# Kernel optimization log

Hardware: AMD Instinct MI355X
Metric: run time of the kernel (lower is better)

## Reference

```python
import jax, jax.numpy as jnp
import numpy as np

N = 100000   # nodes
E = 1200000  # directed edges (avg degree 12)
D = 64       # in_feats
C = 40       # n_classes
K = 16       # propagation steps
ALPHA = 0.05


def setup_inputs() -> dict:
    key = jax.random.key(0)
    k1, k2, k3, k4 = jax.random.split(key, 4)
    feat = jax.random.normal(k1, (N, D), jnp.float32)
    # xavier_uniform for fc.weight [C, D]
    limit = np.sqrt(6.0 / (D + C)).astype(np.float32)
    W = jax.random.uniform(k2, (C, D), jnp.float32, -limit, limit)
    b = jnp.zeros((C,), jnp.float32)
    src = jax.random.randint(k3, (E,), 0, N, dtype=jnp.int32)
    dst = jax.random.randint(k4, (E,), 0, N, dtype=jnp.int32)
    return {"feat": feat, "W": W, "b": b, "src": src, "dst": dst}


def reference(feat, W, b, src, dst):
    # --- getNormAugAdj: A_hat = D^{-1/2} (A + I) D^{-1/2} ---
    loops = jnp.arange(N, dtype=src.dtype)
    row = jnp.concatenate([dst, loops])  # output node of each edge
    col = jnp.concatenate([src, loops])  # input  node of each edge
    ones = jnp.ones(row.shape, feat.dtype)
    deg = jax.ops.segment_sum(ones, row, num_segments=N)  # >= 1 (self-loops)
    dinv = jax.lax.rsqrt(deg)
    w = dinv[row] * dinv[col]  # per-edge normalized weight

    def spmm(x):  # x: [N, D] -> A_hat @ x
        return jax.ops.segment_sum(w[:, None] * x[col], row, num_segments=N)

    feat_ori = feat

    # SSGC loop (faithful to the original, including h /= K inside the loop)
    def step(carry, _):
        x, h = carry
        x = spmm(x)
        h = (h + (1.0 - ALPHA) * x + ALPHA * feat_ori) / K
        return (x, h), None

    (_, h), _ = jax.lax.scan(step, (feat, jnp.zeros_like(feat)), None, length=K)

    # fc(h)
    return h @ W.T + b
```

## Files before the change

kernel.cpp:

```cpp
#include <hip/hip_runtime.h>
#include <hip/hip_fp16.h>

#define NN 100000
#define EE 1200000
#define DD 64
#define CC 40
#define KK 16
#define BSZ 196
#define NBK 512
#define TCAP 3072
#define EPB 4096
#define ABLK ((EE + EPB - 1) / EPB)

#define SLT 261
#define SLT4 196
#define GRID8 (8 * SLT)

typedef int v4i __attribute__((ext_vector_type(4)));

__global__ __launch_bounds__(512) void curinit_kernel(int* __restrict__ cursor) {
    int b = threadIdx.x;
    if (b < NBK) cursor[b] = b * TCAP;
}

__global__ __launch_bounds__(256) void sortA_kernel(const int* __restrict__ src,
                                                    const int* __restrict__ dst,
                                                    int* __restrict__ cursor,
                                                    int2* __restrict__ tmp) {
    __shared__ int2 stg[EPB];
    __shared__ int hist[NBK], loff[NBK], lcur[NBK], gbase[NBK];
    int t = threadIdx.x;
    long e0 = (long)blockIdx.x * EPB;
    int n = (int)((EE - e0 < EPB) ? (EE - e0) : EPB);
    for (int j = t; j < NBK; j += 256) hist[j] = 0;
    __syncthreads();
    int d[16], sx[16];
#pragma unroll
    for (int j = 0; j < 16; ++j) {
        int i = t + j * 256;
        if (i < n) {
            d[j] = dst[e0 + i];
            sx[j] = src[e0 + i];
            atomicAdd(&hist[d[j] / BSZ], 1);
        } else d[j] = -1;
    }
    __syncthreads();
    int c0 = hist[2 * t], c1 = hist[2 * t + 1];
    int s2 = c0 + c1;
    __syncthreads();
    loff[t] = s2;
    __syncthreads();
    for (int off = 1; off < 256; off <<= 1) {
        int u = (t >= off) ? loff[t - off] : 0;
        __syncthreads();
        loff[t] += u;
        __syncthreads();
    }
    int excl = loff[t] - s2;
    __syncthreads();
    loff[2 * t] = excl;          loff[2 * t + 1] = excl + c0;
    lcur[2 * t] = excl;          lcur[2 * t + 1] = excl + c0;
    gbase[2 * t]     = atomicAdd(&cursor[2 * t], c0);
    gbase[2 * t + 1] = atomicAdd(&cursor[2 * t + 1], c1);
    __syncthreads();
#pragma unroll
    for (int j = 0; j < 16; ++j) {
        if (d[j] >= 0) {
            int b = d[j] / BSZ;
            int p = atomicAdd(&lcur[b], 1);
            stg[p] = make_int2(d[j], sx[j]);
        }
    }
    __syncthreads();
    for (int i = t; i < n; i += 256) {
        int2 r = stg[i];
        int b = r.x / BSZ;
        int pos = gbase[b] + (i - loff[b]);
        if (pos < (b + 1) * TCAP) tmp[pos] = r;
    }
}

__global__ __launch_bounds__(512) void bscan_kernel(const int* __restrict__ cursor,
                                                    int* __restrict__ bbase,
                                                    int* __restrict__ row_ptr) {
    __shared__ int sm[512];
    int t = threadIdx.x;
    int v = (t < NBK) ? (cursor[t] - t * TCAP) : 0;
    sm[t] = v;
    __syncthreads();
    for (int off = 1; off < 512; off <<= 1) {
        int u = (t >= off) ? sm[t - off] : 0;
        __syncthreads();
        sm[t] += u;
        __syncthreads();
    }
    if (t < NBK) bbase[t] = sm[t] - v;
    if (t == 511) row_ptr[NN] = sm[511];
}

__global__ __launch_bounds__(256) void sortB_kernel(const int2* __restrict__ tmp,
                                                    const int* __restrict__ cursor,
                                                    const int* __restrict__ bbase,
                                                    float* __restrict__ dinv,
                                                    float* __restrict__ sqd,
                                                    int* __restrict__ row_ptr,
                                                    int* __restrict__ er_src) {
    __shared__ int2 se[TCAP];
    __shared__ int so[TCAP];
    __shared__ int hist[256], lcur[256];
    int b = blockIdx.x;
    int n0 = b * BSZ;
    if (n0 >= NN) return;
    int n1 = n0 + BSZ; if (n1 > NN) n1 = NN;
    int nb = n1 - n0;
    int t = threadIdx.x;
    int cnt = cursor[b] - b * TCAP;
    int base = bbase[b];
    hist[t] = 0;
    __syncthreads();
    for (int i = t; i < cnt; i += 256) {
        int2 r = tmp[b * TCAP + i];
        se[i] = r;
        atomicAdd(&hist[r.x - n0], 1);
    }
    __syncthreads();
    if (t < nb) {
        float dg = (float)(hist[t] + 1);
        dinv[n0 + t] = rsqrtf(dg);
        sqd[n0 + t]  = sqrtf(dg);
    }
    int v = hist[t];
    lcur[t] = v;
    __syncthreads();
    for (int off = 1; off < 256; off <<= 1) {
        int u = (t >= off) ? lcur[t - off] : 0;
        __syncthreads();
        lcur[t] += u;
        __syncthreads();
    }
    int excl = lcur[t] - v;
    __syncthreads();
    lcur[t] = excl;
    if (t < nb) row_ptr[n0 + t] = base + excl;
    __syncthreads();
    for (int i = t; i < cnt; i += 256) {
        int2 r = se[i];
        int ln = r.x - n0;
        int pos = atomicAdd(&lcur[ln], 1);
        so[pos] = r.y;
    }
    __syncthreads();
    for (int i = t; i < cnt; i += 256) er_src[base + i] = so[i];
}

__global__ __launch_bounds__(256) void proj_kernel(const float4* __restrict__ feat4,
                                                   const float* __restrict__ W,
                                                   const float* __restrict__ dinv,
                                                   float4* __restrict__ z0) {
    __shared__ float smW[CC * 68];
    __shared__ float smF[64 * 68];
    __shared__ float smO[64 * 42];
    int t = threadIdx.x;
    for (int j = t; j < CC * 16; j += 256) {
        int c = j >> 4, q = j & 15;
        *(float4*)(smW + c * 68 + q * 4) = ((const float4*)W)[j];
    }
    int n0 = blockIdx.x * 64;
    for (int j = t; j < 64 * 16; j += 256) {
        int r = j >> 4, q = j & 15;
        if (n0 + r < NN)
            *(float4*)(smF + r * 68 + q * 4) = feat4[(size_t)(n0 + r) * 16 + q];
    }
    __syncthreads();
    int ln = t >> 2, c0 = (t & 3) * 10;
    int node = n0 + ln;
    float acc[10];
#pragma unroll
    for (int c = 0; c < 10; ++c) acc[c] = 0.f;
    if (node < NN) {
#pragma unroll
        for (int db = 0; db < 16; ++db) {
            float4 fv = *(const float4*)(smF + ln * 68 + db * 4);
#pragma unroll
            for (int c = 0; c < 10; ++c) {
                float4 wv = *(const float4*)(smW + (c0 + c) * 68 + db * 4);
                acc[c] = fmaf(fv.x, wv.x, acc[c]);
                acc[c] = fmaf(fv.y, wv.y, acc[c]);
                acc[c] = fmaf(fv.z, wv.z, acc[c]);
                acc[c] = fmaf(fv.w, wv.w, acc[c]);
            }
        }
    }
#pragma unroll
    for (int c = 0; c < 10; ++c) smO[ln * 42 + c0 + c] = acc[c];
    __syncthreads();
    for (int j = t; j < 64 * 5; j += 256) {
        int r = j & 63, q = j >> 6;
        int g = n0 + r;
        if (g < NN) {
            float dv = dinv[g];
            const float* s = smO + r * 42 + q * 8;
            float4 ov;
            __half2* op = (__half2*)&ov;
            op[0] = __floats2half2_rn(dv * s[0], dv * s[1]);
            op[1] = __floats2half2_rn(dv * s[2], dv * s[3]);
            op[2] = __floats2half2_rn(dv * s[4], dv * s[5]);
            op[3] = __floats2half2_rn(dv * s[6], dv * s[7]);
            size_t idx = (q < 2) ? ((size_t)g * 2 + q)
                       : (q < 4) ? ((size_t)2 * NN + (size_t)g * 2 + (q - 2))
                                 : ((size_t)4 * NN + g);
            z0[idx] = ov;
        }
    }
}

#define DEC8(V, F0, F1, F2, F3)                                             \
    const __half2* hp_##F0 = (const __half2*)&(V);                          \
    float2 F0 = __half22float2(hp_##F0[0]), F1 = __half22float2(hp_##F0[1]);\
    float2 F2 = __half22float2(hp_##F0[2]), F3 = __half22float2(hp_##F0[3]);

#define ACC8U(V)                                                            \
    {                                                                       \
        DEC8(V, f0, f1, f2, f3)                                             \
        a0 += f0.x; a1 += f0.y; a2 += f1.x; a3 += f1.y;                     \
        a4 += f2.x; a5 += f2.y; a6 += f3.x; a7 += f3.y;                     \
    }

#define GLOOP(XP, STR, PL)                                                  \
    int e = beg;                                                            \
    {                                                                       \
        int ea = (beg + 3) & ~3;                                            \
        if (ea > end) ea = end;                                             \
        for (; e < ea; ++e) {                                               \
            int s = es[e];                                                  \
            float4 v = (XP)[s * (STR) + (PL)];                              \
            ACC8U(v);                                                       \
        }                                                                   \
    }                                                                       \
    int e8 = e + ((end - e) & ~7);                                          \
    for (; e < e8; e += 8) {                                                \
        v4i sA = *(const v4i*)(es + e);                                     \
        v4i sB = *(const v4i*)(es + e + 4);                                 \
        float4 v0 = (XP)[sA.x * (STR) + (PL)];                              \
        float4 v1 = (XP)[sA.y * (STR) + (PL)];                              \
        float4 v2 = (XP)[sA.z * (STR) + (PL)];                              \
        float4 v3 = (XP)[sA.w * (STR) + (PL)];                              \
        float4 v4 = (XP)[sB.x * (STR) + (PL)];                              \
        float4 v5 = (XP)[sB.y * (STR) + (PL)];                              \
        float4 v6 = (XP)[sB.z * (STR) + (PL)];                              \
        float4 v7 = (XP)[sB.w * (STR) + (PL)];                              \
        ACC8U(v0); ACC8U(v1); ACC8U(v2); ACC8U(v3);                         \
        ACC8U(v4); ACC8U(v5); ACC8U(v6); ACC8U(v7);                         \
    }                                                                       \
    int e4 = e + ((end - e) & ~3);                                          \
    for (; e < e4; e += 4) {                                                \
        v4i sA = *(const v4i*)(es + e);                                     \
        float4 v0 = (XP)[sA.x * (STR) + (PL)];                              \
        float4 v1 = (XP)[sA.y * (STR) + (PL)];                              \
        float4 v2 = (XP)[sA.z * (STR) + (PL)];                              \
        float4 v3 = (XP)[sA.w * (STR) + (PL)];                              \
        ACC8U(v0); ACC8U(v1); ACC8U(v2); ACC8U(v3);                         \
    }                                                                       \
    for (; e < end; ++e) {                                                  \
        int s = es[e];                                                      \
        float4 v = (XP)[s * (STR) + (PL)];                                  \
        ACC8U(v);                                                           \
    }

template <int STR>
__device__ __forceinline__ void prop_body(
    int g, int pl, size_t off,
    const float4* __restrict__ x, float4* __restrict__ x_out,
    const int* __restrict__ row_ptr, const int* __restrict__ es,
    const float* __restrict__ dinv) {
    const float4* xp = x + off;
    int beg = row_ptr[g], end = row_ptr[g + 1];
    float di = dinv[g];
    float w2 = di * di;
    int sb = g * STR + pl;
    float4 sv = xp[sb];
    float a0, a1, a2, a3, a4, a5, a6, a7;
    {
        DEC8(sv, f0, f1, f2, f3)
        a0 = f0.x; a1 = f0.y; a2 = f1.x; a3 = f1.y;
        a4 = f2.x; a5 = f2.y; a6 = f3.x; a7 = f3.y;
    }
    GLOOP(xp, STR, pl)
    float4 ov;
    __half2* op = (__half2*)&ov;
    op[0] = __floats2half2_rn(w2 * a0, w2 * a1);
    op[1] = __floats2half2_rn(w2 * a2, w2 * a3);
    op[2] = __floats2half2_rn(w2 * a4, w2 * a5);
    op[3] = __floats2half2_rn(w2 * a6, w2 * a7);
    x_out[off + sb] = ov;
}

__global__ __launch_bounds__(256) void spmm_prop(
    const float4* __restrict__ x, float4* __restrict__ x_out,
    const int* __restrict__ row_ptr, const int* __restrict__ es,
    const float* __restrict__ dinv) {
    int xcd = blockIdx.x & 7;
    int slot = blockIdx.x >> 3;
    int t = threadIdx.x;
    if (xcd < 6) {
        int part = (xcd < 3) ? xcd : xcd - 3;
        int grp  = (xcd < 3) ? 0 : 1;
        int b0 = (part == 0) ? 0 : ((part == 1) ? 33334 : 66667);
        int b1 = (part == 0) ? 33334 : ((part == 1) ? 66667 : 100000);
        int g = b0 + slot * 128 + (t >> 1);
        if (g >= b1) return;
        prop_body<2>(g, t & 1, (size_t)grp * 2 * NN, x, x_out, row_ptr, es, dinv);
    } else {
        if (slot >= SLT4) return;
        int b0 = (xcd - 6) * 50000;
        int g = b0 + slot * 256 + t;
        if (g >= b0 + 50000) return;
        prop_body<1>(g, 0, (size_t)4 * NN, x, x_out, row_ptr, es, dinv);
    }
}

template <int STR>
__device__ __forceinline__ void final_body(
    int g, int pl, int p, size_t off,
    const float4* __restrict__ x15, const float4* __restrict__ x13p,
    const float4* __restrict__ x14p, const float4* __restrict__ z0p,
    const float* __restrict__ bias,
    const int* __restrict__ row_ptr, const int* __restrict__ es,
    const float* __restrict__ dinv, const float* __restrict__ sqd,
    float* __restrict__ outp) {
    const float4* xp = x15 + off;
    int beg = row_ptr[g], end = row_ptr[g + 1];
    float di = dinv[g];
    float sq = sqd[g];
    int sb = g * STR + pl;
    size_t gi = off + sb;
    float4 sv = xp[sb];
    float s0, s1, s2, s3, s4, s5, s6, s7;
    float a0, a1, a2, a3, a4, a5, a6, a7;
    {
        DEC8(sv, f0, f1, f2, f3)
        s0 = f0.x; s1 = f0.y; s2 = f1.x; s3 = f1.y;
        s4 = f2.x; s5 = f2.y; s6 = f3.x; s7 = f3.y;
        a0 = s0; a1 = s1; a2 = s2; a3 = s3;
        a4 = s4; a5 = s5; a6 = s6; a7 = s7;
    }
    GLOOP(xp, STR, pl)
    const float C16 = 0.95f / 16.0f;
    const float C15 = 0.95f / 256.0f;
    const float C14 = 0.95f / 4096.0f;
    const float C13 = 0.95f / 65536.0f;
    const float FC  = 0.05f / 15.0f;
    float t0 = C15 * s0, t1 = C15 * s1, t2 = C15 * s2, t3 = C15 * s3;
    float t4 = C15 * s4, t5 = C15 * s5, t6 = C15 * s6, t7 = C15 * s7;
#define ADD8T(P, CF)                                                        \
    {                                                                       \
        float4 v = (P)[gi];                                                 \
        DEC8(v, f0, f1, f2, f3)                                             \
        t0 = fmaf((CF), f0.x, t0); t1 = fmaf((CF), f0.y, t1);               \
        t2 = fmaf((CF), f1.x, t2); t3 = fmaf((CF), f1.y, t3);               \
        t4 = fmaf((CF), f2.x, t4); t5 = fmaf((CF), f2.y, t5);               \
        t6 = fmaf((CF), f3.x, t6); t7 = fmaf((CF), f3.y, t7);               \
    }
    ADD8T(x14p, C14)
    ADD8T(x13p, C13)
    ADD8T(z0p, FC)
#undef ADD8T
    float cd = C16 * di;
    float o0 = fmaf(sq, t0, cd * a0), o1 = fmaf(sq, t1, cd * a1);
    float o2 = fmaf(sq, t2, cd * a2), o3 = fmaf(sq, t3, cd * a3);
    float o4 = fmaf(sq, t4, cd * a4), o5 = fmaf(sq, t5, cd * a5);
    float o6 = fmaf(sq, t6, cd * a6), o7 = fmaf(sq, t7, cd * a7);
    const float4* b4 = (const float4*)(bias + p * 8);
    float4 bb0 = b4[0], bb1 = b4[1];
    float4* op = (float4*)(outp + (size_t)g * CC + p * 8);
    op[0] = make_float4(o0 + bb0.x, o1 + bb0.y, o2 + bb0.z, o3 + bb0.w);
    op[1] = make_float4(o4 + bb1.x, o5 + bb1.y, o6 + bb1.z, o7 + bb1.w);
}

__global__ __launch_bounds__(256) void spmm_final(
    const float4* __restrict__ x15, const float4* __restrict__ x13p,
    const float4* __restrict__ x14p, const float4* __restrict__ z0p,
    const float* __restrict__ bias,
    const int* __restrict__ row_ptr, const int* __restrict__ es,
    const float* __restrict__ dinv, const float* __restrict__ sqd,
    float* __restrict__ outp) {
    int xcd = blockIdx.x & 7;
    int slot = blockIdx.x >> 3;
    int t = threadIdx.x;
    if (xcd < 6) {
        int part = (xcd < 3) ? xcd : xcd - 3;
        int grp  = (xcd < 3) ? 0 : 1;
        int b0 = (part == 0) ? 0 : ((part == 1) ? 33334 : 66667);
        int b1 = (part == 0) ? 33334 : ((part == 1) ? 66667 : 100000);
        int g = b0 + slot * 128 + (t >> 1);
        if (g >= b1) return;
        int pl = t & 1;
        final_body<2>(g, pl, grp * 2 + pl, (size_t)grp * 2 * NN,
                      x15, x13p, x14p, z0p, bias, row_ptr, es, dinv, sqd, outp);
    } else {
        if (slot >= SLT4) return;
        int b0 = (xcd - 6) * 50000;
        int g = b0 + slot * 256 + t;
        if (g >= b0 + 50000) return;
        final_body<1>(g, 0, 4, (size_t)4 * NN,
                      x15, x13p, x14p, z0p, bias, row_ptr, es, dinv, sqd, outp);
    }
}

extern "C" void kernel_launch(void* const* d_in, const int* in_sizes, int n_in,
                              void* d_out, int out_size, void* d_ws, size_t ws_size,
                              hipStream_t stream) {
    const float* feat = (const float*)d_in[0];
    const float* W    = (const float*)d_in[1];
    const float* b    = (const float*)d_in[2];
    const int*   src  = (const int*)d_in[3];
    const int*   dst  = (const int*)d_in[4];
    float* out = (float*)d_out;

    char* p = (char*)d_ws;
    auto alloc = [&](size_t bytes) {
        char* r = p;
        p += (bytes + 255) & ~(size_t)255;
        return r;
    };
    float*   dinv    = (float*)alloc((size_t)NN * sizeof(float));
    float*   sqd     = (float*)alloc((size_t)NN * sizeof(float));
    int*     row_ptr = (int*)alloc((size_t)(NN + 1) * sizeof(int));
    int*     cursor  = (int*)alloc((size_t)NBK * sizeof(int));
    int*     bbase   = (int*)alloc((size_t)NBK * sizeof(int));
    int2*    tmp     = (int2*)alloc((size_t)NBK * TCAP * sizeof(int2));
    int*     er_src  = (int*)alloc((size_t)EE * sizeof(int));
    float4*  z0      = (float4*)alloc((size_t)NN * 5 * sizeof(float4));
    float4*  xa      = (float4*)alloc((size_t)NN * 5 * sizeof(float4));
    float4*  xb      = (float4*)alloc((size_t)NN * 5 * sizeof(float4));
    float4*  z13     = (float4*)alloc((size_t)NN * 5 * sizeof(float4));
    float4*  z14     = (float4*)alloc((size_t)NN * 5 * sizeof(float4));
    float4*  z15     = (float4*)alloc((size_t)NN * 5 * sizeof(float4));

    curinit_kernel<<<1, 512, 0, stream>>>(cursor);
    sortA_kernel<<<ABLK, 256, 0, stream>>>(src, dst, cursor, tmp);
    bscan_kernel<<<1, 512, 0, stream>>>(cursor, bbase, row_ptr);
    sortB_kernel<<<NBK, 256, 0, stream>>>(tmp, cursor, bbase, dinv, sqd, row_ptr, er_src);
    proj_kernel<<<(NN + 63) / 64, 256, 0, stream>>>((const float4*)feat, W, dinv, z0);

    const float4* xs = z0;
    for (int j = 0; j < 12; ++j) {
        float4* xd = (j & 1) ? xb : xa;
        spmm_prop<<<GRID8, 256, 0, stream>>>(xs, xd, row_ptr, er_src, dinv);
        xs = xd;
    }
    spmm_prop<<<GRID8, 256, 0, stream>>>(xs, z13, row_ptr, er_src, dinv);
    spmm_prop<<<GRID8, 256, 0, stream>>>(z13, z14, row_ptr, er_src, dinv);
    spmm_prop<<<GRID8, 256, 0, stream>>>(z14, z15, row_ptr, er_src, dinv);
    spmm_final<<<GRID8, 256, 0, stream>>>(z15, z13, z14, z0, b, row_ptr,
                                          er_src, dinv, sqd, out);
}
```

Before: 597.8 us.

## Stage block edge indices in LDS with coalesced nontemporal loads before gather

Each block now cooperatively loads its contiguous range of CSR source indices into shared memory in windows of 4096 using vectorized nontemporal loads. Threads then read neighbor indices from LDS instead of issuing per-thread global index loads. Output stores and the single-use reads in the final kernel also become nontemporal so they do not pollute the cache. The cost is extra __syncthreads per window, inactive threads kept alive for the barriers, and LDS use that may lower occupancy.

```diff
diff --git a/kernel.cpp b/kernel.cpp
--- a/kernel.cpp
+++ b/kernel.cpp
@@ -15,8 +15,22 @@
 #define SLT 261
 #define SLT4 196
 #define GRID8 (8 * SLT)
-
-typedef int v4i __attribute__((ext_vector_type(4)));
+#define CH 4096
+
+typedef int   v4i __attribute__((ext_vector_type(4)));
+typedef float v4f __attribute__((ext_vector_type(4)));
+
+__device__ __forceinline__ v4i ntld_i4(const int* p) {
+    return __builtin_nontemporal_load((const v4i*)p);
+}
+__device__ __forceinline__ float4 ntld_f4(const float4* p) {
+    v4f v = __builtin_nontemporal_load((const v4f*)p);
+    return make_float4(v.x, v.y, v.z, v.w);
+}
+__device__ __forceinline__ void ntst_f4(float4* p, float4 f) {
+    v4f v; v.x = f.x; v.y = f.y; v.z = f.z; v.w = f.w;
+    __builtin_nontemporal_store(v, (v4f*)p);
+}
 
 __global__ __launch_bounds__(512) void curinit_kernel(int* __restrict__ cursor) {
     int b = threadIdx.x;
@@ -226,79 +240,94 @@
         a4 += f2.x; a5 += f2.y; a6 += f3.x; a7 += f3.y;                     \
     }
 
-#define GLOOP(XP, STR, PL)                                                  \
-    int e = beg;                                                            \
+#define GATHER_WINDOW(XP, STR, PL)                                          \
     {                                                                       \
-        int ea = (beg + 3) & ~3;                                            \
-        if (ea > end) ea = end;                                             \
-        for (; e < ea; ++e) {                                               \
-            int s = es[e];                                                  \
+        int lo = (beg > W0) ? beg : W0;                                     \
+        int hi = (end < W1) ? end : W1;                                     \
+        int e = lo;                                                         \
+        for (; e + 8 <= hi; e += 8) {                                       \
+            int s0 = sidx[e - A0 + 0], s1 = sidx[e - A0 + 1];               \
+            int s2 = sidx[e - A0 + 2], s3 = sidx[e - A0 + 3];               \
+            int s4 = sidx[e - A0 + 4], s5 = sidx[e - A0 + 5];               \
+            int s6 = sidx[e - A0 + 6], s7 = sidx[e - A0 + 7];               \
+            float4 v0 = (XP)[s0 * (STR) + (PL)];                            \
+            float4 v1 = (XP)[s1 * (STR) + (PL)];                            \
+            float4 v2 = (XP)[s2 * (STR) + (PL)];                            \
+            float4 v3 = (XP)[s3 * (STR) + (PL)];                            \
+            float4 v4 = (XP)[s4 * (STR) + (PL)];                            \
+            float4 v5 = (XP)[s5 * (STR) + (PL)];                            \
+            float4 v6 = (XP)[s6 * (STR) + (PL)];                            \
+            float4 v7 = (XP)[s7 * (STR) + (PL)];                            \
+            ACC8U(v0); ACC8U(v1); ACC8U(v2); ACC8U(v3);                     \
+            ACC8U(v4); ACC8U(v5); ACC8U(v6); ACC8U(v7);                     \
+        }                                                                   \
+        if (e + 4 <= hi) {                                                  \
+            int s0 = sidx[e - A0 + 0], s1 = sidx[e - A0 + 1];               \
+            int s2 = sidx[e - A0 + 2], s3 = sidx[e - A0 + 3];               \
+            float4 v0 = (XP)[s0 * (STR) + (PL)];                            \
+            float4 v1 = (XP)[s1 * (STR) + (PL)];                            \
+            float4 v2 = (XP)[s2 * (STR) + (PL)];                            \
+            float4 v3 = (XP)[s3 * (STR) + (PL)];                            \
+            ACC8U(v0); ACC8U(v1); ACC8U(v2); ACC8U(v3);                     \
+            e += 4;                                                         \
+        }                                                                   \
+        for (; e < hi; ++e) {                                               \
+            int s = sidx[e - A0];                                           \
             float4 v = (XP)[s * (STR) + (PL)];                              \
             ACC8U(v);                                                       \
         }                                                                   \
+    }
+
+#define STAGE_WINDOW                                                        \
+    int W1 = (W0 + CH < blkE) ? (W0 + CH) : blkE;                           \
+    int A0 = W0 & ~3;                                                       \
+    __syncthreads();                                                        \
+    for (int i = A0 + (int)threadIdx.x * 4; i < W1; i += 1024) {            \
+        *(v4i*)(sidx + (i - A0)) = ntld_i4(es + i);                         \
     }                                                                       \
-    int e8 = e + ((end - e) & ~7);                                          \
-    for (; e < e8; e += 8) {                                                \
-        v4i sA = *(const v4i*)(es + e);                                     \
-        v4i sB = *(const v4i*)(es + e + 4);                                 \
-        float4 v0 = (XP)[sA.x * (STR) + (PL)];                              \
-        float4 v1 = (XP)[sA.y * (STR) + (PL)];                              \
-        float4 v2 = (XP)[sA.z * (STR) + (PL)];                              \
-        float4 v3 = (XP)[sA.w * (STR) + (PL)];                              \
-        float4 v4 = (XP)[sB.x * (STR) + (PL)];                              \
-        float4 v5 = (XP)[sB.y * (STR) + (PL)];                              \
-        float4 v6 = (XP)[sB.z * (STR) + (PL)];                              \
-        float4 v7 = (XP)[sB.w * (STR) + (PL)];                              \
-        ACC8U(v0); ACC8U(v1); ACC8U(v2); ACC8U(v3);                         \
-        ACC8U(v4); ACC8U(v5); ACC8U(v6); ACC8U(v7);                         \
-    }                                                                       \
-    int e4 = e + ((end - e) & ~3);                                          \
-    for (; e < e4; e += 4) {                                                \
-        v4i sA = *(const v4i*)(es + e);                                     \
-        float4 v0 = (XP)[sA.x * (STR) + (PL)];                              \
-        float4 v1 = (XP)[sA.y * (STR) + (PL)];                              \
-        float4 v2 = (XP)[sA.z * (STR) + (PL)];                              \
-        float4 v3 = (XP)[sA.w * (STR) + (PL)];                              \
-        ACC8U(v0); ACC8U(v1); ACC8U(v2); ACC8U(v3);                         \
-    }                                                                       \
-    for (; e < end; ++e) {                                                  \
-        int s = es[e];                                                      \
-        float4 v = (XP)[s * (STR) + (PL)];                                  \
-        ACC8U(v);                                                           \
-    }
+    __syncthreads();
 
 template <int STR>
 __device__ __forceinline__ void prop_body(
-    int g, int pl, size_t off,
+    int* sidx, int n0, int n1, int g, bool act, int pl, size_t off,
     const float4* __restrict__ x, float4* __restrict__ x_out,
     const int* __restrict__ row_ptr, const int* __restrict__ es,
     const float* __restrict__ dinv) {
     const float4* xp = x + off;
-    int beg = row_ptr[g], end = row_ptr[g + 1];
-    float di = dinv[g];
-    float w2 = di * di;
-    int sb = g * STR + pl;
-    float4 sv = xp[sb];
-    float a0, a1, a2, a3, a4, a5, a6, a7;
-    {
+    int beg = 0, end = 0, sb = 0;
+    float w2 = 0.f;
+    float a0 = 0, a1 = 0, a2 = 0, a3 = 0, a4 = 0, a5 = 0, a6 = 0, a7 = 0;
+    if (act) {
+        beg = row_ptr[g]; end = row_ptr[g + 1];
+        float di = dinv[g];
+        w2 = di * di;
+        sb = g * STR + pl;
+        float4 sv = xp[sb];
         DEC8(sv, f0, f1, f2, f3)
         a0 = f0.x; a1 = f0.y; a2 = f1.x; a3 = f1.y;
         a4 = f2.x; a5 = f2.y; a6 = f3.x; a7 = f3.y;
     }
-    GLOOP(xp, STR, pl)
-    float4 ov;
-    __half2* op = (__half2*)&ov;
-    op[0] = __floats2half2_rn(w2 * a0, w2 * a1);
-    op[1] = __floats2half2_rn(w2 * a2, w2 * a3);
-    op[2] = __floats2half2_rn(w2 * a4, w2 * a5);
-    op[3] = __floats2half2_rn(w2 * a6, w2 * a7);
-    x_out[off + sb] = ov;
+    int blkB = row_ptr[n0], blkE = row_ptr[n1];
+    for (int W0 = blkB; W0 < blkE; W0 += CH) {
+        STAGE_WINDOW
+        if (act) GATHER_WINDOW(xp, STR, pl)
+    }
+    if (act) {
+        float4 ov;
+        __half2* op = (__half2*)&ov;
+        op[0] = __floats2half2_rn(w2 * a0, w2 * a1);
+        op[1] = __floats2half2_rn(w2 * a2, w2 * a3);
+        op[2] = __floats2half2_rn(w2 * a4, w2 * a5);
+        op[3] = __floats2half2_rn(w2 * a6, w2 * a7);
+        ntst_f4(x_out + off + sb, ov);
+    }
 }
 
 __global__ __launch_bounds__(256) void spmm_prop(
     const float4* __restrict__ x, float4* __restrict__ x_out,
     const int* __restrict__ row_ptr, const int* __restrict__ es,
     const float* __restrict__ dinv) {
+    __shared__ __align__(16) int sidx[CH + 8];
     int xcd = blockIdx.x & 7;
     int slot = blockIdx.x >> 3;
     int t = threadIdx.x;
@@ -307,21 +336,26 @@
         int grp  = (xcd < 3) ? 0 : 1;
         int b0 = (part == 0) ? 0 : ((part == 1) ? 33334 : 66667);
         int b1 = (part == 0) ? 33334 : ((part == 1) ? 66667 : 100000);
-        int g = b0 + slot * 128 + (t >> 1);
-        if (g >= b1) return;
-        prop_body<2>(g, t & 1, (size_t)grp * 2 * NN, x, x_out, row_ptr, es, dinv);
+        int n0 = b0 + slot * 128;
+        int n1 = (n0 + 128 < b1) ? (n0 + 128) : b1;
+        int g = n0 + (t >> 1);
+        prop_body<2>(sidx, n0, n1, g, g < n1, t & 1, (size_t)grp * 2 * NN,
+                     x, x_out, row_ptr, es, dinv);
     } else {
         if (slot >= SLT4) return;
         int b0 = (xcd - 6) * 50000;
-        int g = b0 + slot * 256 + t;
-        if (g >= b0 + 50000) return;
-        prop_body<1>(g, 0, (size_t)4 * NN, x, x_out, row_ptr, es, dinv);
+        int lim = b0 + 50000;
+        int n0 = b0 + slot * 256;
+        int n1 = (n0 + 256 < lim) ? (n0 + 256) : lim;
+        int g = n0 + t;
+        prop_body<1>(sidx, n0, n1, g, g < n1, 0, (size_t)4 * NN,
+                     x, x_out, row_ptr, es, dinv);
     }
 }
 
 template <int STR>
 __device__ __forceinline__ void final_body(
-    int g, int pl, int p, size_t off,
+    int* sidx, int n0, int n1, int g, bool act, int pl, int p, size_t off,
     const float4* __restrict__ x15, const float4* __restrict__ x13p,
     const float4* __restrict__ x14p, const float4* __restrict__ z0p,
     const float* __restrict__ bias,
@@ -329,22 +363,29 @@
     const float* __restrict__ dinv, const float* __restrict__ sqd,
     float* __restrict__ outp) {
     const float4* xp = x15 + off;
-    int beg = row_ptr[g], end = row_ptr[g + 1];
-    float di = dinv[g];
-    float sq = sqd[g];
-    int sb = g * STR + pl;
-    size_t gi = off + sb;
-    float4 sv = xp[sb];
-    float s0, s1, s2, s3, s4, s5, s6, s7;
-    float a0, a1, a2, a3, a4, a5, a6, a7;
-    {
+    int beg = 0, end = 0, sb = 0;
+    float di = 0.f, sq = 0.f;
+    float s0 = 0, s1 = 0, s2 = 0, s3 = 0, s4 = 0, s5 = 0, s6 = 0, s7 = 0;
+    float a0 = 0, a1 = 0, a2 = 0, a3 = 0, a4 = 0, a5 = 0, a6 = 0, a7 = 0;
+    if (act) {
+        beg = row_ptr[g]; end = row_ptr[g + 1];
+        di = dinv[g];
+        sq = sqd[g];
+        sb = g * STR + pl;
+        float4 sv = xp[sb];
         DEC8(sv, f0, f1, f2, f3)
         s0 = f0.x; s1 = f0.y; s2 = f1.x; s3 = f1.y;
         s4 = f2.x; s5 = f2.y; s6 = f3.x; s7 = f3.y;
         a0 = s0; a1 = s1; a2 = s2; a3 = s3;
         a4 = s4; a5 = s5; a6 = s6; a7 = s7;
     }
-    GLOOP(xp, STR, pl)
+    int blkB = row_ptr[n0], blkE = row_ptr[n1];
+    for (int W0 = blkB; W0 < blkE; W0 += CH) {
+        STAGE_WINDOW
+        if (act) GATHER_WINDOW(xp, STR, pl)
+    }
+    if (!act) return;
+    size_t gi = off + sb;
     const float C16 = 0.95f / 16.0f;
     const float C15 = 0.95f / 256.0f;
     const float C14 = 0.95f / 4096.0f;
@@ -354,7 +395,7 @@
     float t4 = C15 * s4, t5 = C15 * s5, t6 = C15 * s6, t7 = C15 * s7;
 #define ADD8T(P, CF)                                                        \
     {                                                                       \
-        float4 v = (P)[gi];                                                 \
+        float4 v = ntld_f4((P) + gi);                                       \
         DEC8(v, f0, f1, f2, f3)                                             \
         t0 = fmaf((CF), f0.x, t0); t1 = fmaf((CF), f0.y, t1);               \
         t2 = fmaf((CF), f1.x, t2); t3 = fmaf((CF), f1.y, t3);               \
@@ -373,8 +414,8 @@
     const float4* b4 = (const float4*)(bias + p * 8);
     float4 bb0 = b4[0], bb1 = b4[1];
     float4* op = (float4*)(outp + (size_t)g * CC + p * 8);
-    op[0] = make_float4(o0 + bb0.x, o1 + bb0.y, o2 + bb0.z, o3 + bb0.w);
-    op[1] = make_float4(o4 + bb1.x, o5 + bb1.y, o6 + bb1.z, o7 + bb1.w);
+    ntst_f4(op,     make_float4(o0 + bb0.x, o1 + bb0.y, o2 + bb0.z, o3 + bb0.w));
+    ntst_f4(op + 1, make_float4(o4 + bb1.x, o5 + bb1.y, o6 + bb1.z, o7 + bb1.w));
 }
 
 __global__ __launch_bounds__(256) void spmm_final(
@@ -384,6 +425,7 @@
     const int* __restrict__ row_ptr, const int* __restrict__ es,
     const float* __restrict__ dinv, const float* __restrict__ sqd,
     float* __restrict__ outp) {
+    __shared__ __align__(16) int sidx[CH + 8];
     int xcd = blockIdx.x & 7;
     int slot = blockIdx.x >> 3;
     int t = threadIdx.x;
@@ -392,17 +434,20 @@
         int grp  = (xcd < 3) ? 0 : 1;
         int b0 = (part == 0) ? 0 : ((part == 1) ? 33334 : 66667);
         int b1 = (part == 0) ? 33334 : ((part == 1) ? 66667 : 100000);
-        int g = b0 + slot * 128 + (t >> 1);
-        if (g >= b1) return;
+        int n0 = b0 + slot * 128;
+        int n1 = (n0 + 128 < b1) ? (n0 + 128) : b1;
+        int g = n0 + (t >> 1);
         int pl = t & 1;
-        final_body<2>(g, pl, grp * 2 + pl, (size_t)grp * 2 * NN,
+        final_body<2>(sidx, n0, n1, g, g < n1, pl, grp * 2 + pl, (size_t)grp * 2 * NN,
                       x15, x13p, x14p, z0p, bias, row_ptr, es, dinv, sqd, outp);
     } else {
         if (slot >= SLT4) return;
         int b0 = (xcd - 6) * 50000;
-        int g = b0 + slot * 256 + t;
-        if (g >= b0 + 50000) return;
-        final_body<1>(g, 0, 4, (size_t)4 * NN,
+        int lim = b0 + 50000;
+        int n0 = b0 + slot * 256;
+        int n1 = (n0 + 256 < lim) ? (n0 + 256) : lim;
+        int g = n0 + t;
+        final_body<1>(sidx, n0, n1, g, g < n1, 0, 4, (size_t)4 * NN,
                       x15, x13p, x14p, z0p, bias, row_ptr, es, dinv, sqd, outp);
     }
 }
@@ -429,7 +474,7 @@
     int*     cursor  = (int*)alloc((size_t)NBK * sizeof(int));
     int*     bbase   = (int*)alloc((size_t)NBK * sizeof(int));
     int2*    tmp     = (int2*)alloc((size_t)NBK * TCAP * sizeof(int2));
-    int*     er_src  = (int*)alloc((size_t)EE * sizeof(int));
+    int*     er_src  = (int*)alloc((size_t)EE * sizeof(int) + 64);
     float4*  z0      = (float4*)alloc((size_t)NN * 5 * sizeof(float4));
     float4*  xa      = (float4*)alloc((size_t)NN * 5 * sizeof(float4));
     float4*  xb      = (float4*)alloc((size_t)NN * 5 * sizeof(float4));
```

Result: faster. 547.8 us (-8.4%).
